# Optimization experiments

Hardware: AMD Instinct MI355X
Metric: run time of the kernel (lower is better)

Reference implementation:

```python
import jax, jax.numpy as jnp
import numpy as np

B, C_IN, H, W = 16, 256, 64, 64
D, K = 128, 1024  # embed_dim, nb_entries


def setup_inputs() -> dict:
    key = jax.random.key(0)
    k1, k2, k3, k4 = jax.random.split(key, 4)
    x = jax.random.normal(k1, (B, C_IN, H, W), dtype=jnp.float32)
    conv_w = jax.random.normal(k2, (C_IN, D), dtype=jnp.float32) * 0.05
    conv_b = jax.random.normal(k3, (D,), dtype=jnp.float32) * 0.05
    embed = jax.random.normal(k4, (D, K), dtype=jnp.float32)
    return {"x": x, "conv_w": conv_w, "conv_b": conv_b, "embed": embed}


def reference(x, conv_w, conv_b, embed):
    # 1x1 conv == per-pixel matmul; go straight to NHWC layout.
    z = jnp.einsum('bchw,cd->bhwd', x, conv_w) + conv_b        # [B,H,W,D]
    flat = z.reshape(-1, D)                                     # [N,D]
    # Squared-euclidean distances to codebook columns (||f||^2 - 2 f.E + ||e||^2).
    dist = (jnp.sum(flat * flat, axis=1, keepdims=True)
            - 2.0 * (flat @ embed)
            + jnp.sum(embed * embed, axis=0, keepdims=True))    # [N,K]
    embed_ind = jnp.argmin(dist, axis=1)                        # [N] int
    embed_ind = embed_ind.reshape(B, H, W)
    quantize = jnp.take(embed.T, embed_ind, axis=0)             # [B,H,W,D] gather
    diff = jnp.mean((jax.lax.stop_gradient(quantize) - z) ** 2)
    quantize = z + jax.lax.stop_gradient(quantize - z)          # straight-through
    return quantize.transpose(0, 3, 1, 2), diff, embed_ind
```

## Files before the change

kernel.cpp:

```cpp
#include <hip/hip_runtime.h>

typedef __attribute__((ext_vector_type(4))) float f32x4;
typedef __attribute__((ext_vector_type(8))) short bf16x8;

constexpr int CIN = 256;
constexpr int D   = 128;
constexpr int K   = 1024;
constexpr int HW  = 4096;
constexpr int MT  = 128;
constexpr int DIFF_OFF = 8388608;
constexpr int IDX_OFF  = 8388609;

__device__ float g_scratch[16 + K];
__device__ __align__(16) uint4 g_efrags[64 * 8 * 64];
__device__ __align__(16) uint4 g_wfrags[8 * 8 * 3 * 64];
__device__ __align__(16) float g_embedT[K * D];

__device__ inline unsigned short f2bf(float f) {
    unsigned u = __float_as_uint(f);
    u = u + 0x7fff + ((u >> 16) & 1);
    return (unsigned short)(u >> 16);
}
__device__ inline float bf2f(unsigned short h) {
    return __uint_as_float(((unsigned)h) << 16);
}
__device__ inline void split3(float v, short& a, short& b, short& c) {
    unsigned short h = f2bf(v); float r1 = v - bf2f(h);
    unsigned short m = f2bf(r1); float r2 = r1 - bf2f(m);
    a = (short)h; b = (short)m; c = (short)f2bf(r2);
}

__global__ void vq_init(const float* __restrict__ embed) {
    int k = blockIdx.x * 256 + threadIdx.x;
    if (k == 0) g_scratch[0] = 0.0f;
    if (k < K) {
        float s = 0.0f;
        for (int d = 0; d < D; ++d) { float v = embed[d * K + k]; s += v * v; }
        g_scratch[16 + k] = s;
    }
}

__global__ void vq_prep2(const float* __restrict__ embed) {
    __shared__ float tile[32][33];
    int kb = blockIdx.x >> 2, db = blockIdx.x & 3;
    int t = threadIdx.x, tk = t & 31, td = t >> 5;
    #pragma unroll
    for (int dd = 0; dd < 4; ++dd)
        tile[td * 4 + dd][tk] = embed[(size_t)(db * 32 + td * 4 + dd) * K + kb * 32 + tk];
    __syncthreads();
    #pragma unroll
    for (int dd = 0; dd < 4; ++dd)
        g_embedT[(size_t)(kb * 32 + td * 4 + dd) * D + db * 32 + tk] = tile[tk][td * 4 + dd];
}

__global__ void vq_prep(const float* __restrict__ embed) {
    int kt = blockIdx.x >> 2, dc = blockIdx.x & 3;
    int l  = threadIdx.x;
    int k  = kt * 16 + (l & 15);
    int d0 = dc * 32 + (l >> 4) * 8;
    unsigned short hi[8], lo[8];
    #pragma unroll
    for (int j = 0; j < 8; ++j) {
        float v = embed[(size_t)(d0 + j) * K + k];
        hi[j] = f2bf(v);
        lo[j] = f2bf(v - bf2f(hi[j]));
    }
    uint4 H, L;
    H.x = (unsigned)hi[0] | ((unsigned)hi[1] << 16);
    H.y = (unsigned)hi[2] | ((unsigned)hi[3] << 16);
    H.z = (unsigned)hi[4] | ((unsigned)hi[5] << 16);
    H.w = (unsigned)hi[6] | ((unsigned)hi[7] << 16);
    L.x = (unsigned)lo[0] | ((unsigned)lo[1] << 16);
    L.y = (unsigned)lo[2] | ((unsigned)lo[3] << 16);
    L.z = (unsigned)lo[4] | ((unsigned)lo[5] << 16);
    L.w = (unsigned)lo[6] | ((unsigned)lo[7] << 16);
    g_efrags[(kt * 8 + dc * 2 + 0) * 64 + l] = H;
    g_efrags[(kt * 8 + dc * 2 + 1) * 64 + l] = L;
}

__global__ void vq_prepw(const float* __restrict__ conv_w) {
    int cb = blockIdx.x >> 3, db = blockIdx.x & 7, l = threadIdx.x;
    int c0 = cb * 32 + (l >> 4) * 8, d = db * 16 + (l & 15);
    short s1[8], s2[8], s3[8];
    #pragma unroll
    for (int j = 0; j < 8; ++j)
        split3(conv_w[(size_t)(c0 + j) * D + d], s1[j], s2[j], s3[j]);
    uint4 P[3];
    #pragma unroll
    for (int s = 0; s < 3; ++s) {
        const short* sp = s == 0 ? s1 : s == 1 ? s2 : s3;
        P[s].x = (unsigned)(unsigned short)sp[0] | ((unsigned)(unsigned short)sp[1] << 16);
        P[s].y = (unsigned)(unsigned short)sp[2] | ((unsigned)(unsigned short)sp[3] << 16);
        P[s].z = (unsigned)(unsigned short)sp[4] | ((unsigned)(unsigned short)sp[5] << 16);
        P[s].w = (unsigned)(unsigned short)sp[6] | ((unsigned)(unsigned short)sp[7] << 16);
        g_wfrags[((cb * 8 + db) * 3 + s) * 64 + l] = P[s];
    }
}

#define MFMA(a, bb, c) __builtin_amdgcn_mfma_f32_16x16x32_bf16(a, bb, c, 0, 0, 0)

__global__ __launch_bounds__(256, 2) void vq_main(
    const float* __restrict__ x, const float* __restrict__ conv_b,
    float* __restrict__ out)
{
    __shared__ uint4 ebuf[4096];
    __shared__ float e2_s[K];
    __shared__ float tbuf[4 * 16 * 36];
    __shared__ int   ks_s[MT];
    __shared__ float red_s[4];

    const int t    = threadIdx.x;
    const int lane = t & 63;
    const int w    = t >> 6;
    const int wg   = blockIdx.x;
    const int n0   = wg * MT;
    const int b    = n0 >> 12;
    const int hw0  = n0 & 4095;
    const int pxb  = w * 32;
    const int lp   = lane & 15;
    const int lg   = lane >> 4;

    for (int k = t; k < K; k += 256) e2_s[k] = g_scratch[16 + k];

    f32x4 Cz[2][8];
    #pragma unroll
    for (int db = 0; db < 8; ++db) {
        float bv = conv_b[db * 16 + lp];
        Cz[0][db] = (f32x4){bv, bv, bv, bv};
        Cz[1][db] = Cz[0][db];
    }
    {
        const float* xl = x + (size_t)b * CIN * HW + (size_t)(lg * 8) * HW
                          + hw0 + pxb + lp;
        for (int cb = 0; cb < 8; ++cb) {
            bf16x8 X1[2], X2[2], X3[2];
            #pragma unroll
            for (int rb = 0; rb < 2; ++rb) {
                float v[8];
                #pragma unroll
                for (int j = 0; j < 8; ++j)
                    v[j] = xl[(size_t)(cb * 32 + j) * HW + rb * 16];
                #pragma unroll
                for (int j = 0; j < 8; ++j) {
                    short a, bb, c;
                    split3(v[j], a, bb, c);
                    X1[rb][j] = a; X2[rb][j] = bb; X3[rb][j] = c;
                }
            }
            #pragma unroll
            for (int db = 0; db < 8; ++db) {
                bf16x8 W1 = *(const bf16x8*)&g_wfrags[((cb * 8 + db) * 3 + 0) * 64 + lane];
                bf16x8 W2 = *(const bf16x8*)&g_wfrags[((cb * 8 + db) * 3 + 1) * 64 + lane];
                bf16x8 W3 = *(const bf16x8*)&g_wfrags[((cb * 8 + db) * 3 + 2) * 64 + lane];
                Cz[0][db] = MFMA(X1[0], W1, Cz[0][db]);
                Cz[1][db] = MFMA(X1[1], W1, Cz[1][db]);
                Cz[0][db] = MFMA(X1[0], W2, Cz[0][db]);
                Cz[1][db] = MFMA(X1[1], W2, Cz[1][db]);
                Cz[0][db] = MFMA(X2[0], W1, Cz[0][db]);
                Cz[1][db] = MFMA(X2[1], W1, Cz[1][db]);
                Cz[0][db] = MFMA(X1[0], W3, Cz[0][db]);
                Cz[1][db] = MFMA(X1[1], W3, Cz[1][db]);
                Cz[0][db] = MFMA(X2[0], W2, Cz[0][db]);
                Cz[1][db] = MFMA(X2[1], W2, Cz[1][db]);
                Cz[0][db] = MFMA(X3[0], W1, Cz[0][db]);
                Cz[1][db] = MFMA(X3[1], W1, Cz[1][db]);
            }
        }
    }

    bf16x8 A2h[2][4], A2l[2][4];
    {
        float* tb = tbuf + w * 576;
        #pragma unroll
        for (int rb = 0; rb < 2; ++rb) {
            #pragma unroll
            for (int dc = 0; dc < 4; ++dc) {
                #pragma unroll
                for (int h = 0; h < 2; ++h)
                    #pragma unroll
                    for (int r = 0; r < 4; ++r)
                        tb[(lg * 4 + r) * 36 + h * 16 + lp] = Cz[rb][dc * 2 + h][r];
                asm volatile("s_waitcnt lgkmcnt(0)" ::: "memory");
                f32x4 a0 = *(const f32x4*)&tb[lp * 36 + lg * 8];
                f32x4 a1 = *(const f32x4*)&tb[lp * 36 + lg * 8 + 4];
                #pragma unroll
                for (int j = 0; j < 8; ++j) {
                    float zv = -2.0f * (j < 4 ? a0[j] : a1[j - 4]);
                    unsigned short hb = f2bf(zv);
                    A2h[rb][dc][j] = (short)hb;
                    A2l[rb][dc][j] = (short)f2bf(zv - bf2f(hb));
                }
                asm volatile("s_waitcnt lgkmcnt(0)" ::: "memory");
            }
        }
    }

    const uint4* gfr = g_efrags;
    {
        uint4 tmp[8];
        #pragma unroll
        for (int i = 0; i < 8; ++i) tmp[i] = gfr[i * 256 + t];
        #pragma unroll
        for (int i = 0; i < 8; ++i) ebuf[i * 256 + t] = tmp[i];
    }
    __syncthreads();

    float v1[8], v2[8]; int i1[8], i2[8];
    #pragma unroll
    for (int q = 0; q < 8; ++q) { v1[q] = 3.4e38f; v2[q] = 3.4e38f; i1[q] = 0; i2[q] = 0; }

    for (int c = 0; c < 16; ++c) {
        uint4 tmp[8];
        if (c < 15) {
            #pragma unroll
            for (int i = 0; i < 8; ++i) tmp[i] = gfr[(c + 1) * 2048 + i * 256 + t];
        }
        const bf16x8* eb = (const bf16x8*)&ebuf[(c & 1) * 2048];
        #pragma unroll
        for (int ktl = 0; ktl < 4; ++ktl) {
            int kt = c * 4 + ktl;
            bf16x8 Bh[4], Bl[4];
            #pragma unroll
            for (int dc = 0; dc < 4; ++dc) {
                Bh[dc] = eb[(ktl * 8 + dc * 2 + 0) * 64 + lane];
                Bl[dc] = eb[(ktl * 8 + dc * 2 + 1) * 64 + lane];
            }
            float e2v = e2_s[kt * 16 + lp];
            f32x4 C0 = (f32x4){e2v, e2v, e2v, e2v};
            f32x4 C1 = C0;
            #pragma unroll
            for (int dc = 0; dc < 4; ++dc) {
                C0 = MFMA(A2h[0][dc], Bh[dc], C0);
                C1 = MFMA(A2h[1][dc], Bh[dc], C1);
                C0 = MFMA(A2l[0][dc], Bh[dc], C0);
                C1 = MFMA(A2l[1][dc], Bh[dc], C1);
                C0 = MFMA(A2h[0][dc], Bl[dc], C0);
                C1 = MFMA(A2h[1][dc], Bl[dc], C1);
            }
            int kk = kt * 16 + lp;
            #pragma unroll
            for (int rb = 0; rb < 2; ++rb) {
                f32x4 C = rb ? C1 : C0;
                #pragma unroll
                for (int r = 0; r < 4; ++r) {
                    int q = rb * 4 + r;
                    float s = C[r];
                    bool lt1 = s < v1[q], lt2 = s < v2[q];
                    v2[q] = lt1 ? v1[q] : (lt2 ? s  : v2[q]);
                    i2[q] = lt1 ? i1[q] : (lt2 ? kk : i2[q]);
                    v1[q] = lt1 ? s  : v1[q];
                    i1[q] = lt1 ? kk : i1[q];
                }
            }
        }
        if (c < 15) {
            #pragma unroll
            for (int i = 0; i < 8; ++i) ebuf[((c + 1) & 1) * 2048 + i * 256 + t] = tmp[i];
        }
        __syncthreads();
    }

    #pragma unroll
    for (int off = 1; off < 16; off <<= 1) {
        #pragma unroll
        for (int q = 0; q < 8; ++q) {
            float b1 = __shfl_xor(v1[q], off); int bi1 = __shfl_xor(i1[q], off);
            float b2 = __shfl_xor(v2[q], off); int bi2 = __shfl_xor(i2[q], off);
            bool bf = (b1 < v1[q]) || (b1 == v1[q] && bi1 < i1[q]);
            float cv = bf ? v1[q] : b1;  int ci = bf ? i1[q] : bi1;
            float wv = bf ? b2 : v2[q];  int wi = bf ? bi2 : i2[q];
            v1[q] = bf ? b1 : v1[q];     i1[q] = bf ? bi1 : i1[q];
            bool c2 = (cv < wv) || (cv == wv && ci < wi);
            v2[q] = c2 ? cv : wv;        i2[q] = c2 ? ci : wi;
        }
    }

    float dacc = 0.0f;
    #pragma unroll
    for (int q = 0; q < 8; ++q) {
        const int rb = q >> 2, r = q & 3;
        const int k1 = i1[q], k2 = i2[q];
        float s1 = 0.0f, s2 = 0.0f;
        #pragma unroll
        for (int db = 0; db < 8; ++db) {
            float zv = Cz[rb][db][r];
            s1 += zv * g_embedT[(size_t)k1 * D + db * 16 + lp];
            s2 += zv * g_embedT[(size_t)k2 * D + db * 16 + lp];
        }
        #pragma unroll
        for (int off = 1; off < 16; off <<= 1) {
            s1 += __shfl_xor(s1, off);
            s2 += __shfl_xor(s2, off);
        }
        float d1 = e2_s[k1] - 2.0f * s1;
        float d2 = e2_s[k2] - 2.0f * s2;
        bool p2 = (d2 < d1) || (d2 == d1 && k2 < k1);
        int ks = p2 ? k2 : k1;
        #pragma unroll
        for (int db = 0; db < 8; ++db) {
            float zv = Cz[rb][db][r];
            float qv = g_embedT[(size_t)ks * D + db * 16 + lp];
            float df = qv - zv;
            dacc += df * df;
        }
        if (lp == 0) {
            int px = pxb + rb * 16 + lg * 4 + r;
            ks_s[px] = ks;
            out[IDX_OFF + n0 + px] = (float)ks;
        }
    }
    #pragma unroll
    for (int off = 1; off <= 32; off <<= 1) dacc += __shfl_xor(dacc, off);
    if (lane == 0) red_s[w] = dacc;
    __syncthreads();

    {
        int px = t & 127, half = t >> 7;
        int ks = ks_s[px];
        const f32x4* ep = (const f32x4*)&g_embedT[(size_t)ks * D + half * 64];
        float* ob = out + (size_t)b * D * HW + hw0 + px;
        #pragma unroll
        for (int d4 = 0; d4 < 16; ++d4) {
            f32x4 q4 = ep[d4];
            int d = half * 64 + d4 * 4;
            #pragma unroll
            for (int cc = 0; cc < 4; ++cc)
                ob[(size_t)(d + cc) * HW] = q4[cc];
        }
    }
    if (t == 0) atomicAdd(&g_scratch[0], red_s[0] + red_s[1] + red_s[2] + red_s[3]);
}

__global__ void vq_final(float* __restrict__ out) {
    out[DIFF_OFF] = g_scratch[0] / 8388608.0f;
}

extern "C" void kernel_launch(void* const* d_in, const int* in_sizes, int n_in,
                              void* d_out, int out_size, void* d_ws, size_t ws_size,
                              hipStream_t stream) {
    const float* x      = (const float*)d_in[0];
    const float* conv_w = (const float*)d_in[1];
    const float* conv_b = (const float*)d_in[2];
    const float* embed  = (const float*)d_in[3];
    float* out = (float*)d_out;

    vq_init  <<<4,   256, 0, stream>>>(embed);
    vq_prep2 <<<128, 256, 0, stream>>>(embed);
    vq_prep  <<<256, 64,  0, stream>>>(embed);
    vq_prepw <<<64,  64,  0, stream>>>(conv_w);
    vq_main  <<<512, 256, 0, stream>>>(x, conv_b, out);
    vq_final <<<1,   1,   0, stream>>>(out);
}
```

Before: 104.2 us.

## Stage weight and codebook fragments into LDS via direct global-to-LDS async loads

The conv stage now double-buffers the pre-split weight fragments in LDS using global_load_lds, instead of every wave reading them from global memory for each MFMA. The codebook prefetch in the distance loop also switches from register staging to direct global-to-LDS loads, which frees registers and drops the explicit LDS store pass. s_setprio is raised around the MFMA blocks. The cost is extra barriers and vmcnt waits in the conv loop, plus a dependence on the LDS destination layout matching the fragment order.

```diff
diff --git a/kernel.cpp b/kernel.cpp
--- a/kernel.cpp
+++ b/kernel.cpp
@@ -28,6 +28,13 @@
     unsigned short h = f2bf(v); float r1 = v - bf2f(h);
     unsigned short m = f2bf(r1); float r2 = r1 - bf2f(m);
     a = (short)h; b = (short)m; c = (short)f2bf(r2);
+}
+
+__device__ inline void gload_lds16(const uint4* g, uint4* l) {
+    __builtin_amdgcn_global_load_lds(
+        (const __attribute__((address_space(1))) unsigned int*)g,
+        (__attribute__((address_space(3))) unsigned int*)l,
+        16, 0, 0);
 }
 
 __global__ void vq_init(const float* __restrict__ embed) {
@@ -85,15 +92,15 @@
     #pragma unroll
     for (int j = 0; j < 8; ++j)
         split3(conv_w[(size_t)(c0 + j) * D + d], s1[j], s2[j], s3[j]);
-    uint4 P[3];
     #pragma unroll
     for (int s = 0; s < 3; ++s) {
         const short* sp = s == 0 ? s1 : s == 1 ? s2 : s3;
-        P[s].x = (unsigned)(unsigned short)sp[0] | ((unsigned)(unsigned short)sp[1] << 16);
-        P[s].y = (unsigned)(unsigned short)sp[2] | ((unsigned)(unsigned short)sp[3] << 16);
-        P[s].z = (unsigned)(unsigned short)sp[4] | ((unsigned)(unsigned short)sp[5] << 16);
-        P[s].w = (unsigned)(unsigned short)sp[6] | ((unsigned)(unsigned short)sp[7] << 16);
-        g_wfrags[((cb * 8 + db) * 3 + s) * 64 + l] = P[s];
+        uint4 P;
+        P.x = (unsigned)(unsigned short)sp[0] | ((unsigned)(unsigned short)sp[1] << 16);
+        P.y = (unsigned)(unsigned short)sp[2] | ((unsigned)(unsigned short)sp[3] << 16);
+        P.z = (unsigned)(unsigned short)sp[4] | ((unsigned)(unsigned short)sp[5] << 16);
+        P.w = (unsigned)(unsigned short)sp[6] | ((unsigned)(unsigned short)sp[7] << 16);
+        g_wfrags[((cb * 8 + db) * 3 + s) * 64 + l] = P;
     }
 }
 
@@ -103,7 +110,7 @@
     const float* __restrict__ x, const float* __restrict__ conv_b,
     float* __restrict__ out)
 {
-    __shared__ uint4 ebuf[4096];
+    __shared__ __align__(16) uint4 ebuf[4096];
     __shared__ float e2_s[K];
     __shared__ float tbuf[4 * 16 * 36];
     __shared__ int   ks_s[MT];
@@ -130,28 +137,43 @@
         Cz[1][db] = Cz[0][db];
     }
     {
+        #pragma unroll
+        for (int i = 0; i < 6; ++i)
+            gload_lds16(&g_wfrags[(w * 6 + i) * 64 + lane], &ebuf[(w * 6 + i) * 64]);
+        asm volatile("s_waitcnt vmcnt(0)" ::: "memory");
+        __syncthreads();
+
         const float* xl = x + (size_t)b * CIN * HW + (size_t)(lg * 8) * HW
                           + hw0 + pxb + lp;
         for (int cb = 0; cb < 8; ++cb) {
+            float v[2][8];
+            #pragma unroll
+            for (int rb = 0; rb < 2; ++rb)
+                #pragma unroll
+                for (int j = 0; j < 8; ++j)
+                    v[rb][j] = xl[(size_t)(cb * 32 + j) * HW + rb * 16];
+            if (cb < 7) {
+                const uint4* wsrc = g_wfrags + (size_t)(cb + 1) * 1536;
+                uint4* wdst = ebuf + ((cb + 1) & 1) * 1536;
+                #pragma unroll
+                for (int i = 0; i < 6; ++i)
+                    gload_lds16(&wsrc[(w * 6 + i) * 64 + lane], &wdst[(w * 6 + i) * 64]);
+            }
             bf16x8 X1[2], X2[2], X3[2];
             #pragma unroll
-            for (int rb = 0; rb < 2; ++rb) {
-                float v[8];
-                #pragma unroll
-                for (int j = 0; j < 8; ++j)
-                    v[j] = xl[(size_t)(cb * 32 + j) * HW + rb * 16];
+            for (int rb = 0; rb < 2; ++rb)
                 #pragma unroll
                 for (int j = 0; j < 8; ++j) {
                     short a, bb, c;
-                    split3(v[j], a, bb, c);
+                    split3(v[rb][j], a, bb, c);
                     X1[rb][j] = a; X2[rb][j] = bb; X3[rb][j] = c;
                 }
-            }
+            const uint4* wb = ebuf + (cb & 1) * 1536;
             #pragma unroll
             for (int db = 0; db < 8; ++db) {
-                bf16x8 W1 = *(const bf16x8*)&g_wfrags[((cb * 8 + db) * 3 + 0) * 64 + lane];
-                bf16x8 W2 = *(const bf16x8*)&g_wfrags[((cb * 8 + db) * 3 + 1) * 64 + lane];
-                bf16x8 W3 = *(const bf16x8*)&g_wfrags[((cb * 8 + db) * 3 + 2) * 64 + lane];
+                bf16x8 W1 = *(const bf16x8*)&wb[(db * 3 + 0) * 64 + lane];
+                bf16x8 W2 = *(const bf16x8*)&wb[(db * 3 + 1) * 64 + lane];
+                bf16x8 W3 = *(const bf16x8*)&wb[(db * 3 + 2) * 64 + lane];
                 Cz[0][db] = MFMA(X1[0], W1, Cz[0][db]);
                 Cz[1][db] = MFMA(X1[1], W1, Cz[1][db]);
                 Cz[0][db] = MFMA(X1[0], W2, Cz[0][db]);
@@ -165,6 +187,8 @@
                 Cz[0][db] = MFMA(X3[0], W1, Cz[0][db]);
                 Cz[1][db] = MFMA(X3[1], W1, Cz[1][db]);
             }
+            asm volatile("s_waitcnt vmcnt(0)" ::: "memory");
+            __syncthreads();
         }
     }
 
@@ -197,23 +221,24 @@
 
     const uint4* gfr = g_efrags;
     {
-        uint4 tmp[8];
-        #pragma unroll
-        for (int i = 0; i < 8; ++i) tmp[i] = gfr[i * 256 + t];
-        #pragma unroll
-        for (int i = 0; i < 8; ++i) ebuf[i * 256 + t] = tmp[i];
-    }
-    __syncthreads();
+        #pragma unroll
+        for (int i = 0; i < 8; ++i)
+            gload_lds16(&gfr[(w * 8 + i) * 64 + lane], &ebuf[(w * 8 + i) * 64]);
+        asm volatile("s_waitcnt vmcnt(0)" ::: "memory");
+        __syncthreads();
+    }
 
     float v1[8], v2[8]; int i1[8], i2[8];
     #pragma unroll
     for (int q = 0; q < 8; ++q) { v1[q] = 3.4e38f; v2[q] = 3.4e38f; i1[q] = 0; i2[q] = 0; }
 
     for (int c = 0; c < 16; ++c) {
-        uint4 tmp[8];
         if (c < 15) {
-            #pragma unroll
-            for (int i = 0; i < 8; ++i) tmp[i] = gfr[(c + 1) * 2048 + i * 256 + t];
+            const uint4* esrc = gfr + (size_t)(c + 1) * 2048;
+            uint4* edst = ebuf + ((c + 1) & 1) * 2048;
+            #pragma unroll
+            for (int i = 0; i < 8; ++i)
+                gload_lds16(&esrc[(w * 8 + i) * 64 + lane], &edst[(w * 8 + i) * 64]);
         }
         const bf16x8* eb = (const bf16x8*)&ebuf[(c & 1) * 2048];
         #pragma unroll
@@ -228,6 +253,7 @@
             float e2v = e2_s[kt * 16 + lp];
             f32x4 C0 = (f32x4){e2v, e2v, e2v, e2v};
             f32x4 C1 = C0;
+            __builtin_amdgcn_s_setprio(1);
             #pragma unroll
             for (int dc = 0; dc < 4; ++dc) {
                 C0 = MFMA(A2h[0][dc], Bh[dc], C0);
@@ -237,6 +263,7 @@
                 C0 = MFMA(A2h[0][dc], Bl[dc], C0);
                 C1 = MFMA(A2h[1][dc], Bl[dc], C1);
             }
+            __builtin_amdgcn_s_setprio(0);
             int kk = kt * 16 + lp;
             #pragma unroll
             for (int rb = 0; rb < 2; ++rb) {
@@ -253,10 +280,7 @@
                 }
             }
         }
-        if (c < 15) {
-            #pragma unroll
-            for (int i = 0; i < 8; ++i) ebuf[((c + 1) & 1) * 2048 + i * 256 + t] = tmp[i];
-        }
+        if (c < 15) asm volatile("s_waitcnt vmcnt(0)" ::: "memory");
         __syncthreads();
     }
 
```

Result: no change. 102.2 us (-1.9%).
